# Kernel optimization log

Hardware: AMD Instinct MI355X
Metric: run time of the kernel (lower is better)

Reference implementation:

```python
import jax, jax.numpy as jnp
import numpy as np

N_WIRES = 4
N_LAYERS = 2
BSZ = 4096


def _gate(p):
    # combined single-qubit gate RX(p2) @ RZ(p1) @ RY(p0)  (RY applied first)
    a, b, c = p[0] * 0.5, p[1] * 0.5, p[2] * 0.5
    ca, sa = jnp.cos(a), jnp.sin(a)
    ry = jnp.stack([jnp.stack([ca, -sa]), jnp.stack([sa, ca])]).astype(jnp.complex64)
    eb = (jnp.cos(b) - 1j * jnp.sin(b)).astype(jnp.complex64)  # e^{-i b}
    zero = jnp.zeros((), jnp.complex64)
    rz = jnp.stack([jnp.stack([eb, zero]), jnp.stack([zero, jnp.conj(eb)])])
    cc, sc = jnp.cos(c), jnp.sin(c)
    rx = jnp.stack([jnp.stack([cc + 0j, -1j * sc]), jnp.stack([-1j * sc, cc + 0j])]).astype(jnp.complex64)
    return rx @ rz @ ry


def _apply1(state, U, w):
    # state: (N,2,2,2,2); apply 2x2 gate U on wire w
    s = jnp.moveaxis(state, w + 1, 4)
    s = jnp.einsum('nijka,ba->nijkb', s, U)
    return jnp.moveaxis(s, 4, w + 1)


def _cnot(state, c, t):
    s = jnp.moveaxis(state, (c + 1, t + 1), (1, 2))
    s = jnp.stack([s[:, 0], jnp.flip(s[:, 1], axis=1)], axis=1)
    return jnp.moveaxis(s, (1, 2), (c + 1, t + 1))


def _quanv(x, params):
    bsz = x.shape[0]
    # extract 2x2 patches in the same order as the torch loop:
    # [x[r,c], x[r,c+1], x[r+1,c], x[r+1,c+1]], row-major over (r,c)
    p = x.reshape(bsz, 14, 2, 14, 2).transpose(0, 1, 3, 2, 4).reshape(bsz * 196, 4)
    h = p * 0.5
    v = jnp.stack([jnp.cos(h), jnp.sin(h)], axis=-1).astype(jnp.complex64)  # (N,4,2): RY(patch)|0>
    state = jnp.einsum('na,nb,nc,nd->nabcd', v[:, 0], v[:, 1], v[:, 2], v[:, 3])
    for l in range(N_LAYERS):
        for w in range(N_WIRES):
            state = _apply1(state, _gate(params[l, w]), w)
        for w in range(N_WIRES - 1):
            state = _cnot(state, w, w + 1)
        state = _cnot(state, N_WIRES - 1, 0)
    probs = state.real ** 2 + state.imag ** 2  # (N,2,2,2,2)
    z = jnp.array([1.0, -1.0], jnp.float32)
    exps = []
    for w in range(N_WIRES):
        axes = tuple(i for i in range(1, 5) if i != w + 1)
        exps.append(probs.sum(axes) @ z)  # <Z_w>, shape (N,)
    # (N,4) -> (bsz, 196, 4) -> (bsz, 784), patch-major / wire-minor like torch.cat
    return jnp.stack(exps, axis=-1).reshape(bsz, 196 * N_WIRES)


def setup_inputs() -> dict:
    key = jax.random.key(0)
    k1, k2 = jax.random.split(key)
    x = jax.random.uniform(k1, (BSZ, 28, 28), dtype=jnp.float32)
    params = jax.random.normal(k2, (N_LAYERS, N_WIRES, 3), dtype=jnp.float32)
    return {"x": x, "params": params}


def reference(x, params):
    return _quanv(x, params)
```

## Files before the change

### kernel.cpp

```cpp
#include <hip/hip_runtime.h>


typedef _Float16 f16;
typedef _Float16 half8 __attribute__((ext_vector_type(8)));
typedef float f4 __attribute__((ext_vector_type(4)));

#define PK2(a, b) __builtin_bit_cast(float, __builtin_amdgcn_cvt_pkrtz((a), (b)))
#define RDL(x, g) __builtin_bit_cast(float, __builtin_amdgcn_readlane(__builtin_bit_cast(int, (x)), (g)))

__device__ __forceinline__ float2 cmulf(float2 a, float2 b) {
    return make_float2(fmaf(a.x, b.x, -(a.y * b.y)),
                       fmaf(a.x, b.y,   a.y * b.x));
}

__global__ __launch_bounds__(64, 4) void quanv_kernel(
        const float* __restrict__ x,
        const float* __restrict__ params,
        float* __restrict__ out)
{
    __shared__ __align__(16) f16 Wt[32][40];
    __shared__ __align__(16) unsigned char SB[64 * 80];

    const int l = threadIdx.x;
    const int gid = blockIdx.x * 64 + l;

    const int n = gid / 196;
    const int p = gid - n * 196;
    const int r = p / 14;
    const int c = p - r * 14;
    const float* xb = x + n * 784 + r * 56 + c * 2;
    const float2 top = *(const float2*)(xb);
    const float2 bot = *(const float2*)(xb + 28);

    const float* pg = params + (l & 7) * 3;
    const float ha = 0.5f * pg[0], hb = 0.5f * pg[1], hc = 0.5f * pg[2];
    const float sa = __sinf(ha), ca = __cosf(ha);
    const float sb = __sinf(hb), cb = __cosf(hb);
    const float sc = __sinf(hc), cx = __cosf(hc);
    const float gx = cx*ca*cb + sc*sa*sb;
    const float gy = -(cx*ca*sb + sc*sa*cb);
    const float gz = sc*ca*sb - cx*sa*cb;
    const float gw = cx*sa*sb - sc*ca*cb;
    float Ax[8], Ay[8], Bx[8], By[8];
#pragma unroll
    for (int g = 0; g < 8; ++g) {
        Ax[g] = RDL(gx, g); Ay[g] = RDL(gy, g);
        Bx[g] = RDL(gz, g); By[g] = RDL(gw, g);
    }

    const unsigned long long IDX1P = 0x497a2f1c85b6e3d0ULL;
    const unsigned long long INV1P = 0xa3185ce7d46f2b90ULL;
    const int mE = l & 15;
    const int kN = (int)((INV1P >> (mE * 4)) & 15);
#pragma unroll
    for (int ii = 0; ii < 4; ++ii) {
        const int iE = (l >> 4) + 4 * ii;
        const int jN = (int)((IDX1P >> (iE * 4)) & 15);
        float2 e = make_float2(1.f, 0.f);
#pragma unroll
        for (int w = 0; w < 4; ++w) {
            const int jb = (jN >> (3 - w)) & 1;
            const int kb = (kN >> (3 - w)) & 1;
            const float ux = jb ? (kb ?  Ax[4+w] : -Bx[4+w]) : (kb ? Bx[4+w] : Ax[4+w]);
            const float uy = jb ? (kb ? -Ay[4+w] :  By[4+w]) : (kb ? By[4+w] : Ay[4+w]);
            e = cmulf(e, make_float2(ux, uy));
        }
        *(float*)&Wt[iE][2 * mE]      = PK2(e.x, -e.y);
        *(float*)&Wt[16 + iE][2 * mE] = PK2(e.y,  e.x);
    }

    const float pw0 = 0.5f * top.x, pw1 = 0.5f * top.y;
    const float pw2 = 0.5f * bot.x, pw3 = 0.5f * bot.y;
    const float pwv[4] = {pw0, pw1, pw2, pw3};
    float2 wv[4][2];
#pragma unroll
    for (int w = 0; w < 4; ++w) {
        const float cw = __cosf(pwv[w]);
        const float sw = __sinf(pwv[w]);
        wv[w][0] = make_float2(fmaf(Bx[w], sw,  Ax[w] * cw), fmaf( By[w], sw, Ay[w] * cw));
        wv[w][1] = make_float2(fmaf(Ax[w], sw, -Bx[w] * cw), fmaf(-Ay[w], sw, By[w] * cw));
    }

    float2 ab[4], cd[4];
#pragma unroll
    for (int i = 0; i < 2; ++i)
#pragma unroll
        for (int j = 0; j < 2; ++j) {
            ab[i * 2 + j] = cmulf(wv[0][i], wv[1][j]);
            cd[i * 2 + j] = cmulf(wv[2][i], wv[3][j]);
        }
    float sd[16];
#pragma unroll
    for (int hi = 0; hi < 4; ++hi)
#pragma unroll
        for (int lo = 0; lo < 4; ++lo) {
            const float2 sv = cmulf(ab[hi], cd[lo]);
            sd[hi * 4 + lo] = PK2(sv.x, sv.y);
        }

    f16* st = (f16*)(SB + l * 80);
    *(float4*)(st)      = make_float4(sd[0],  sd[1],  sd[2],  sd[3]);
    *(float4*)(st + 8)  = make_float4(sd[4],  sd[5],  sd[6],  sd[7]);
    *(float4*)(st + 16) = make_float4(sd[8],  sd[9],  sd[10], sd[11]);
    *(float4*)(st + 24) = make_float4(sd[12], sd[13], sd[14], sd[15]);

    __syncthreads();

    const int q = l >> 4, c16 = l & 15;
    const half8 b0 = *(const half8*)&Wt[c16][q * 8];
    const half8 b1 = *(const half8*)&Wt[16 + c16][q * 8];
    const f4 zf4 = {0.f, 0.f, 0.f, 0.f};
    f4 d0[4], d1[4];
#pragma unroll
    for (int m = 0; m < 4; ++m) {
        const half8 am = *(const half8*)(SB + (m * 16 + c16) * 80 + q * 16);
        d0[m] = __builtin_amdgcn_mfma_f32_16x16x32_f16(am, b0, zf4, 0, 0, 0);
        d1[m] = __builtin_amdgcn_mfma_f32_16x16x32_f16(am, b1, zf4, 0, 0, 0);
    }

    float* prb = (float*)SB;
#pragma unroll
    for (int m = 0; m < 4; ++m)
#pragma unroll
        for (int reg = 0; reg < 4; ++reg) {
            const float pv = fmaf(d0[m][reg], d0[m][reg], d1[m][reg] * d1[m][reg]);
            prb[(m * 16 + q * 4 + reg) * 20 + c16] = pv;
        }

    const float4 p0 = *(const float4*)(prb + l * 20);
    const float4 p1 = *(const float4*)(prb + l * 20 + 4);
    const float4 p2 = *(const float4*)(prb + l * 20 + 8);
    const float4 p3 = *(const float4*)(prb + l * 20 + 12);

    const float t00 = p0.x + p0.y + p0.z + p0.w;
    const float t01 = p1.x + p1.y + p1.z + p1.w;
    const float t10 = p2.x + p2.y + p2.z + p2.w;
    const float t11 = p3.x + p3.y + p3.z + p3.w;
    const float e0 = (t00 + t01) - (t10 + t11);
    const float e1 = (t00 - t01) + (t10 - t11);

    const float u00 = p0.x + p1.x + p2.x + p3.x;
    const float u01 = p0.y + p1.y + p2.y + p3.y;
    const float u10 = p0.z + p1.z + p2.z + p3.z;
    const float u11 = p0.w + p1.w + p2.w + p3.w;
    const float e2 = (u00 + u01) - (u10 + u11);
    const float e3 = (u00 - u01) + (u10 - u11);

    *(float4*)(out + gid * 4) = make_float4(e0, e1, e2, e3);
}

extern "C" void kernel_launch(void* const* d_in, const int* in_sizes, int n_in,
                              void* d_out, int out_size, void* d_ws, size_t ws_size,
                              hipStream_t stream) {
    const float* x      = (const float*)d_in[0];
    const float* params = (const float*)d_in[1];
    float* out = (float*)d_out;

    const int npatch = 4096 * 196;
    quanv_kernel<<<npatch / 64, 64, 0, stream>>>(x, params, out);
}
```

Measured before the change: 76.57 us.

## Use 256-thread blocks with shared gate table and per-wave MFMA scratch

```diff
diff --git a/kernel.cpp b/kernel.cpp
--- a/kernel.cpp
+++ b/kernel.cpp
@@ -6,23 +6,23 @@
 typedef float f4 __attribute__((ext_vector_type(4)));
 
 #define PK2(a, b) __builtin_bit_cast(float, __builtin_amdgcn_cvt_pkrtz((a), (b)))
-#define RDL(x, g) __builtin_bit_cast(float, __builtin_amdgcn_readlane(__builtin_bit_cast(int, (x)), (g)))
 
 __device__ __forceinline__ float2 cmulf(float2 a, float2 b) {
     return make_float2(fmaf(a.x, b.x, -(a.y * b.y)),
                        fmaf(a.x, b.y,   a.y * b.x));
 }
 
-__global__ __launch_bounds__(64, 4) void quanv_kernel(
+__global__ __launch_bounds__(256, 4) void quanv_kernel(
         const float* __restrict__ x,
         const float* __restrict__ params,
         float* __restrict__ out)
 {
+    __shared__ float4 Gs[8];
     __shared__ __align__(16) f16 Wt[32][40];
-    __shared__ __align__(16) unsigned char SB[64 * 80];
+    __shared__ __align__(16) unsigned char SB[4][5120];
 
-    const int l = threadIdx.x;
-    const int gid = blockIdx.x * 64 + l;
+    const int t = threadIdx.x;
+    const int gid = blockIdx.x * 256 + t;
 
     const int n = gid / 196;
     const int p = gid - n * 196;
@@ -32,53 +32,49 @@
     const float2 top = *(const float2*)(xb);
     const float2 bot = *(const float2*)(xb + 28);
 
-    const float* pg = params + (l & 7) * 3;
-    const float ha = 0.5f * pg[0], hb = 0.5f * pg[1], hc = 0.5f * pg[2];
-    const float sa = __sinf(ha), ca = __cosf(ha);
-    const float sb = __sinf(hb), cb = __cosf(hb);
-    const float sc = __sinf(hc), cx = __cosf(hc);
-    const float gx = cx*ca*cb + sc*sa*sb;
-    const float gy = -(cx*ca*sb + sc*sa*cb);
-    const float gz = sc*ca*sb - cx*sa*cb;
-    const float gw = cx*sa*sb - sc*ca*cb;
-    float Ax[8], Ay[8], Bx[8], By[8];
-#pragma unroll
-    for (int g = 0; g < 8; ++g) {
-        Ax[g] = RDL(gx, g); Ay[g] = RDL(gy, g);
-        Bx[g] = RDL(gz, g); By[g] = RDL(gw, g);
+    if (t < 8) {
+        const float* pg = params + t * 3;
+        const float ha = 0.5f * pg[0], hb = 0.5f * pg[1], hc = 0.5f * pg[2];
+        const float sa = __sinf(ha), ca = __cosf(ha);
+        const float sb = __sinf(hb), cb = __cosf(hb);
+        const float sc = __sinf(hc), cx = __cosf(hc);
+        Gs[t] = make_float4(cx*ca*cb + sc*sa*sb,
+                            -(cx*ca*sb + sc*sa*cb),
+                            sc*ca*sb - cx*sa*cb,
+                            cx*sa*sb - sc*ca*cb);
     }
+    __syncthreads();
 
-    const unsigned long long IDX1P = 0x497a2f1c85b6e3d0ULL;
-    const unsigned long long INV1P = 0xa3185ce7d46f2b90ULL;
-    const int mE = l & 15;
-    const int kN = (int)((INV1P >> (mE * 4)) & 15);
-#pragma unroll
-    for (int ii = 0; ii < 4; ++ii) {
-        const int iE = (l >> 4) + 4 * ii;
+    {
+        const unsigned long long IDX1P = 0x497a2f1c85b6e3d0ULL;
+        const unsigned long long INV1P = 0xa3185ce7d46f2b90ULL;
+        const int iE = t >> 4;
+        const int mE = t & 15;
         const int jN = (int)((IDX1P >> (iE * 4)) & 15);
+        const int kN = (int)((INV1P >> (mE * 4)) & 15);
         float2 e = make_float2(1.f, 0.f);
 #pragma unroll
         for (int w = 0; w < 4; ++w) {
+            const float4 g = Gs[4 + w];
             const int jb = (jN >> (3 - w)) & 1;
             const int kb = (kN >> (3 - w)) & 1;
-            const float ux = jb ? (kb ?  Ax[4+w] : -Bx[4+w]) : (kb ? Bx[4+w] : Ax[4+w]);
-            const float uy = jb ? (kb ? -Ay[4+w] :  By[4+w]) : (kb ? By[4+w] : Ay[4+w]);
+            const float ux = jb ? (kb ?  g.x : -g.z) : (kb ? g.z : g.x);
+            const float uy = jb ? (kb ? -g.y :  g.w) : (kb ? g.w : g.y);
             e = cmulf(e, make_float2(ux, uy));
         }
         *(float*)&Wt[iE][2 * mE]      = PK2(e.x, -e.y);
         *(float*)&Wt[16 + iE][2 * mE] = PK2(e.y,  e.x);
     }
 
-    const float pw0 = 0.5f * top.x, pw1 = 0.5f * top.y;
-    const float pw2 = 0.5f * bot.x, pw3 = 0.5f * bot.y;
-    const float pwv[4] = {pw0, pw1, pw2, pw3};
+    const float pwv[4] = {0.5f * top.x, 0.5f * top.y, 0.5f * bot.x, 0.5f * bot.y};
     float2 wv[4][2];
 #pragma unroll
     for (int w = 0; w < 4; ++w) {
         const float cw = __cosf(pwv[w]);
         const float sw = __sinf(pwv[w]);
-        wv[w][0] = make_float2(fmaf(Bx[w], sw,  Ax[w] * cw), fmaf( By[w], sw, Ay[w] * cw));
-        wv[w][1] = make_float2(fmaf(Ax[w], sw, -Bx[w] * cw), fmaf(-Ay[w], sw, By[w] * cw));
+        const float4 g = Gs[w];
+        wv[w][0] = make_float2(fmaf(g.z, sw,  g.x * cw), fmaf( g.w, sw, g.y * cw));
+        wv[w][1] = make_float2(fmaf(g.x, sw, -g.z * cw), fmaf(-g.y, sw, g.w * cw));
     }
 
     float2 ab[4], cd[4];
@@ -98,7 +94,12 @@
             sd[hi * 4 + lo] = PK2(sv.x, sv.y);
         }
 
-    f16* st = (f16*)(SB + l * 80);
+    const int l   = t & 63;
+    const int wid = t >> 6;
+    const int q   = l >> 4;
+    const int c16 = l & 15;
+
+    f16* st = (f16*)(SB[wid] + l * 80);
     *(float4*)(st)      = make_float4(sd[0],  sd[1],  sd[2],  sd[3]);
     *(float4*)(st + 8)  = make_float4(sd[4],  sd[5],  sd[6],  sd[7]);
     *(float4*)(st + 16) = make_float4(sd[8],  sd[9],  sd[10], sd[11]);
@@ -106,19 +107,18 @@
 
     __syncthreads();
 
-    const int q = l >> 4, c16 = l & 15;
     const half8 b0 = *(const half8*)&Wt[c16][q * 8];
     const half8 b1 = *(const half8*)&Wt[16 + c16][q * 8];
     const f4 zf4 = {0.f, 0.f, 0.f, 0.f};
     f4 d0[4], d1[4];
 #pragma unroll
     for (int m = 0; m < 4; ++m) {
-        const half8 am = *(const half8*)(SB + (m * 16 + c16) * 80 + q * 16);
+        const half8 am = *(const half8*)(SB[wid] + (m * 16 + c16) * 80 + q * 16);
         d0[m] = __builtin_amdgcn_mfma_f32_16x16x32_f16(am, b0, zf4, 0, 0, 0);
         d1[m] = __builtin_amdgcn_mfma_f32_16x16x32_f16(am, b1, zf4, 0, 0, 0);
     }
 
-    float* prb = (float*)SB;
+    float* prb = (float*)SB[wid];
 #pragma unroll
     for (int m = 0; m < 4; ++m)
 #pragma unroll
@@ -157,5 +157,5 @@
     float* out = (float*)d_out;
 
     const int npatch = 4096 * 196;
-    quanv_kernel<<<npatch / 64, 64, 0, stream>>>(x, params, out);
+    quanv_kernel<<<npatch / 256, 256, 0, stream>>>(x, params, out);
 }
```

Measured after the change: 71.63 us. -6.5%, faster.
